# Performance work log

Hardware: AMD Instinct MI355X
Metric: run time of the kernel (lower is better)

The kernel has to match this reference:

```python
import jax, jax.numpy as jnp
import numpy as np

N, NFEAT, NHID, NCLASS = 8192, 128, 128, 40


def _init(key, shape, fan_in):
    return jax.random.normal(key, shape, jnp.float32) / np.sqrt(fan_in).astype(np.float32)


def setup_inputs() -> dict:
    ks = jax.random.split(jax.random.key(0), 8)
    return {
        "x": jax.random.normal(ks[0], (N, NFEAT), jnp.float32),
        # dense normalized adjacency: row-stochastic-ish positive matrix
        "adj": jax.random.uniform(ks[1], (N, N), jnp.float32) * (2.0 / N),
        "W_emb": _init(ks[2], (NFEAT, NHID), NFEAT),
        "b_emb": jnp.zeros((NHID,), jnp.float32),
        "W_gc1": _init(ks[3], (NHID, NHID), NHID),
        "b_gc1": jnp.zeros((NHID,), jnp.float32),
        "W_e": _init(ks[4], (2 * NHID, NHID), 2 * NHID),
        "b_e": jnp.zeros((NHID,), jnp.float32),
        "W_gc2": _init(ks[5], (NHID, NCLASS), NHID),
        "b_gc2": jnp.zeros((NCLASS,), jnp.float32),
        "fully_connected_graph": 1,  # unused by forward (passed but never read)
    }


def reference(x, adj, W_emb, b_emb, W_gc1, b_gc1, W_e, b_e, W_gc2, b_gc2,
              fully_connected_graph):
    nhid = W_emb.shape[1]
    # x = self.emb(x)
    h = x @ W_emb + b_emb  # [N, nhid]

    # Edge branch. Original materializes edge_feat[i*N+j] = concat(h[i], h[j])
    # ([N*N, 2*nhid]) then GraphConvolution_edge: support = edge_feat @ W_e,
    # reshaped [N, N, nhid], aggregated x_e[i] = sum_j adj[i,j] * support[i,j] + b_e.
    # Algebraically identical fused form (same math, no O(N^2*nhid) tensor):
    #   support[i,j] = h[i] @ W_e[:nhid] + h[j] @ W_e[nhid:]
    #   x_e[i] = deg[i] * (h[i] @ W_e_src) + (adj @ (h @ W_e_dst))[i] + b_e
    s_src = h @ W_e[:nhid]   # [N, nhid]
    s_dst = h @ W_e[nhid:]   # [N, nhid]
    deg = adj.sum(axis=1, keepdims=True)  # [N, 1] row sums
    x_e = deg * s_src + adj @ s_dst + b_e  # [N, nhid]

    # Node branch: gc1 -> relu -> dropout(eval: identity) -> gc2 -> log_softmax
    h1 = jax.nn.relu(adj @ (h @ W_gc1) + b_gc1)       # [N, nhid]
    logits = adj @ (h1 @ W_gc2) + b_gc2               # [N, nclass]
    out = jax.nn.log_softmax(logits, axis=1)
    return out, x_e
```

## Files before the change

kernel.cpp:

```cpp
#include <hip/hip_runtime.h>

#define DI __device__ __forceinline__

using f32x4  = __attribute__((ext_vector_type(4))) float;
using bf16x8 = __attribute__((ext_vector_type(8))) __bf16;
using u16x4  = __attribute__((ext_vector_type(4))) unsigned short;
using u32x4  = __attribute__((ext_vector_type(4))) unsigned int;

constexpr int NNODE = 8192;

DI unsigned short f2bf(float f) {
    unsigned int u = __builtin_bit_cast(unsigned int, f);
    u += 0x7fffu + ((u >> 16) & 1u);
    return (unsigned short)(u >> 16);
}
DI float bf2f(unsigned short s) {
    return __builtin_bit_cast(float, (unsigned int)s << 16);
}

DI int swz256(int r, int cb) { return r * 256 + (cb ^ ((r & 15) << 4)); }
DI int swz128(int r, int cb) { return r * 128 + (cb ^ ((r & 7) << 4)); }

__global__ void prep_w(const float* __restrict__ W_emb, const float* __restrict__ W_e,
                       const float* __restrict__ W_gc1, const float* __restrict__ W_gc2,
                       unsigned short* __restrict__ WembT_hi, unsigned short* __restrict__ WembT_lo,
                       unsigned short* __restrict__ WcatT_hi, unsigned short* __restrict__ WcatT_lo,
                       unsigned short* __restrict__ Wg2T_hi, unsigned short* __restrict__ Wg2T_lo)
{
    int gid = blockIdx.x * 256 + threadIdx.x;
    if (gid >= 576 * 128) return;
    int k = gid & 127, n = gid >> 7;
    float v;
    unsigned short *dh, *dl;
    if (n < 128) {
        v = W_emb[k * 128 + n];
        dh = WembT_hi + n * 128 + k; dl = WembT_lo + n * 128 + k;
    } else if (n < 512) {
        int m = n - 128;
        if (m < 128)      v = W_e[k * 128 + m];
        else if (m < 256) v = W_e[(k + 128) * 128 + (m - 128)];
        else              v = W_gc1[k * 128 + (m - 256)];
        dh = WcatT_hi + m * 128 + k; dl = WcatT_lo + m * 128 + k;
    } else {
        int c = n - 512;
        v = (c < 40) ? W_gc2[k * 40 + c] : 0.f;
        dh = Wg2T_hi + c * 128 + k; dl = Wg2T_lo + c * 128 + k;
    }
    unsigned short hi = f2bf(v);
    *dh = hi;
    *dl = f2bf(v - bf2f(hi));
}

template<int NCHUNK, int AKIND, int OUTKIND>
__global__ __launch_bounds__(256) void small_gemm(
    const float* __restrict__ Af32,
    const unsigned short* __restrict__ A_hi, const unsigned short* __restrict__ A_lo,
    const unsigned short* __restrict__ Bt_hi, const unsigned short* __restrict__ Bt_lo,
    const float* __restrict__ bias,
    unsigned short* __restrict__ out_hi, unsigned short* __restrict__ out_lo,
    float* __restrict__ out_s,
    unsigned short* __restrict__ out_t)
{
    __shared__ unsigned short Ah[64 * 128], Al[64 * 128];
    __shared__ unsigned short Bh[NCHUNK * 128], Bl[NCHUNK * 128];
    char* Ahc = (char*)Ah; char* Alc = (char*)Al;
    char* Bhc = (char*)Bh; char* Blc = (char*)Bl;

    const int tid = threadIdx.x;
    const int r0 = blockIdx.x * 64;
    const int n0 = blockIdx.y * NCHUNK;

    if constexpr (AKIND == 0) {
        #pragma unroll
        for (int p = 0; p < 8; ++p) {
            int idx = tid + 256 * p, r = idx >> 5, c4 = idx & 31;
            f32x4 v = *(const f32x4*)(Af32 + (size_t)(r0 + r) * 128 + c4 * 4);
            u16x4 ph, pl;
            #pragma unroll
            for (int j = 0; j < 4; ++j) {
                unsigned short hi = f2bf(v[j]);
                ph[j] = hi; pl[j] = f2bf(v[j] - bf2f(hi));
            }
            *(u16x4*)(Ahc + swz256(r, c4 * 8)) = ph;
            *(u16x4*)(Alc + swz256(r, c4 * 8)) = pl;
        }
    } else {
        #pragma unroll
        for (int p = 0; p < 4; ++p) {
            int idx = tid + 256 * p, r = idx >> 4, c = idx & 15;
            u32x4 vh = *(const u32x4*)(A_hi + (size_t)(r0 + r) * 128 + c * 8);
            u32x4 vl = *(const u32x4*)(A_lo + (size_t)(r0 + r) * 128 + c * 8);
            *(u32x4*)(Ahc + swz256(r, c * 16)) = vh;
            *(u32x4*)(Alc + swz256(r, c * 16)) = vl;
        }
    }
    #pragma unroll
    for (int p = 0; p < NCHUNK / 16; ++p) {
        int idx = tid + 256 * p, r = idx >> 4, c = idx & 15;
        u32x4 vh = *(const u32x4*)(Bt_hi + (size_t)(n0 + r) * 128 + c * 8);
        u32x4 vl = *(const u32x4*)(Bt_lo + (size_t)(n0 + r) * 128 + c * 8);
        *(u32x4*)(Bhc + swz256(r, c * 16)) = vh;
        *(u32x4*)(Blc + swz256(r, c * 16)) = vl;
    }
    __syncthreads();

    const int lane = tid & 63, wid = tid >> 6;
    const int lrow = lane & 15, lkb = (lane >> 4) * 16;
    constexpr int FN = NCHUNK / 16;
    f32x4 acc[FN];
    #pragma unroll
    for (int i = 0; i < FN; ++i) acc[i] = f32x4{0.f, 0.f, 0.f, 0.f};

    const int arow = wid * 16 + lrow;
    #pragma unroll
    for (int kk = 0; kk < 4; ++kk) {
        bf16x8 ah = *(const bf16x8*)(Ahc + swz256(arow, kk * 64 + lkb));
        bf16x8 al = *(const bf16x8*)(Alc + swz256(arow, kk * 64 + lkb));
        #pragma unroll
        for (int nf = 0; nf < FN; ++nf) {
            bf16x8 bh = *(const bf16x8*)(Bhc + swz256(nf * 16 + lrow, kk * 64 + lkb));
            bf16x8 bl = *(const bf16x8*)(Blc + swz256(nf * 16 + lrow, kk * 64 + lkb));
            acc[nf] = __builtin_amdgcn_mfma_f32_16x16x32_bf16(ah, bh, acc[nf], 0, 0, 0);
            acc[nf] = __builtin_amdgcn_mfma_f32_16x16x32_bf16(ah, bl, acc[nf], 0, 0, 0);
            acc[nf] = __builtin_amdgcn_mfma_f32_16x16x32_bf16(al, bh, acc[nf], 0, 0, 0);
        }
    }

    const int rowb = r0 + wid * 16 + ((lane >> 4) << 2);
    #pragma unroll
    for (int nf = 0; nf < FN; ++nf) {
        const int col = n0 + nf * 16 + lrow;
        if constexpr (OUTKIND == 0) {
            float bv = bias[col];
            #pragma unroll
            for (int j = 0; j < 4; ++j) {
                float v = acc[nf][j] + bv;
                unsigned short hi = f2bf(v);
                out_hi[(size_t)(rowb + j) * 128 + col] = hi;
                out_lo[(size_t)(rowb + j) * 128 + col] = f2bf(v - bf2f(hi));
            }
        } else if constexpr (OUTKIND == 1) {
            if (col < 128) {
                #pragma unroll
                for (int j = 0; j < 4; ++j)
                    out_s[(size_t)(rowb + j) * 128 + col] = acc[nf][j];
            } else {
                u16x4 pk = { f2bf(acc[nf][0]), f2bf(acc[nf][1]), f2bf(acc[nf][2]), f2bf(acc[nf][3]) };
                *(u16x4*)(out_t + (size_t)(col - 128) * NNODE + rowb) = pk;
            }
        } else {
            u16x4 pk = { f2bf(acc[nf][0]), f2bf(acc[nf][1]), f2bf(acc[nf][2]), f2bf(acc[nf][3]) };
            *(u16x4*)(out_t + (size_t)col * NNODE + rowb) = pk;
        }
    }
}

template<int NCOLS, bool DEG>
__global__ __launch_bounds__(512) void adj_gemm(
    const float* __restrict__ adj,
    const unsigned short* __restrict__ Bt,
    float* __restrict__ Tpart,
    float* __restrict__ deg)
{
    __shared__ unsigned short A_lds[2][64 * 64];
    __shared__ unsigned short B_lds[2][NCOLS * 64];

    const int tid = threadIdx.x;
    const int r0 = blockIdx.x * 64;
    const int ks = blockIdx.y;
    constexpr int KLEN = NNODE / 2;
    constexpr int NT = KLEN / 64;
    const int kbase = ks * KLEN;

    constexpr int NB = NCOLS / 64;
    f32x4 areg[2];
    u32x4 breg[NB];
    float dsum0 = 0.f, dsum1 = 0.f;
    const int ar0 = tid >> 4, ac4 = tid & 15;

    const int lane = tid & 63, wid = tid >> 6;
    constexpr int FM = (NCOLS == 256) ? 2 : 1;
    constexpr int FN = (NCOLS == 256) ? 4 : 2;
    const int wr = (NCOLS == 256) ? (wid >> 2) : (wid >> 1);
    const int wc = (NCOLS == 256) ? (wid & 3) : (wid & 1);
    const int row_w = wr * FM * 16, col_w = wc * FN * 16;
    const int lrow = lane & 15, lkb = (lane >> 4) * 16;

    f32x4 acc[FM][FN];
    #pragma unroll
    for (int fm = 0; fm < FM; ++fm)
        #pragma unroll
        for (int fn = 0; fn < FN; ++fn) acc[fm][fn] = f32x4{0.f, 0.f, 0.f, 0.f};

    auto loadG = [&](int t) {
        const int kt = kbase + t * 64;
        #pragma unroll
        for (int p = 0; p < 2; ++p) {
            areg[p] = *(const f32x4*)(adj + (size_t)(r0 + ar0 + 32 * p) * NNODE + kt + ac4 * 4);
            if (DEG) {
                float s = areg[p][0] + areg[p][1] + areg[p][2] + areg[p][3];
                if (p == 0) dsum0 += s; else dsum1 += s;
            }
        }
        #pragma unroll
        for (int p = 0; p < NB; ++p) {
            const int idx = tid + 512 * p, n = idx >> 3, c = idx & 7;
            breg[p] = *(const u32x4*)(Bt + (size_t)n * NNODE + kt + c * 8);
        }
    };
    auto storeL = [&](int buf) {
        char* Ac = (char*)(A_lds[buf]);
        char* Bc = (char*)(B_lds[buf]);
        #pragma unroll
        for (int p = 0; p < 2; ++p) {
            u16x4 pk = { f2bf(areg[p][0]), f2bf(areg[p][1]), f2bf(areg[p][2]), f2bf(areg[p][3]) };
            *(u16x4*)(Ac + swz128(ar0 + 32 * p, ac4 * 8)) = pk;
        }
        #pragma unroll
        for (int p = 0; p < NB; ++p) {
            const int idx = tid + 512 * p, n = idx >> 3, c = idx & 7;
            *(u32x4*)(Bc + swz128(n, c * 16)) = breg[p];
        }
    };

    loadG(0);
    storeL(0);
    for (int t = 0; t < NT; ++t) {
        if (t + 1 < NT) loadG(t + 1);
        __syncthreads();
        const char* Ac = (const char*)(A_lds[t & 1]);
        const char* Bc = (const char*)(B_lds[t & 1]);
        #pragma unroll
        for (int kk = 0; kk < 2; ++kk) {
            bf16x8 a[FM], b[FN];
            #pragma unroll
            for (int fm = 0; fm < FM; ++fm)
                a[fm] = *(const bf16x8*)(Ac + swz128(row_w + fm * 16 + lrow, kk * 64 + lkb));
            #pragma unroll
            for (int fn = 0; fn < FN; ++fn)
                b[fn] = *(const bf16x8*)(Bc + swz128(col_w + fn * 16 + lrow, kk * 64 + lkb));
            #pragma unroll
            for (int fm = 0; fm < FM; ++fm)
                #pragma unroll
                for (int fn = 0; fn < FN; ++fn)
                    acc[fm][fn] = __builtin_amdgcn_mfma_f32_16x16x32_bf16(a[fm], b[fn], acc[fm][fn], 0, 0, 0);
        }
        if (t + 1 < NT) storeL((t + 1) & 1);
    }

    float* outp = Tpart + (size_t)ks * NNODE * NCOLS;
    #pragma unroll
    for (int fm = 0; fm < FM; ++fm) {
        const int grow0 = r0 + row_w + fm * 16 + ((lane >> 4) << 2);
        #pragma unroll
        for (int fn = 0; fn < FN; ++fn) {
            const int gcol = col_w + fn * 16 + lrow;
            #pragma unroll
            for (int j = 0; j < 4; ++j)
                outp[(size_t)(grow0 + j) * NCOLS + gcol] = acc[fm][fn][j];
        }
    }

    if (DEG) {
        __syncthreads();
        float* sc = (float*)(&A_lds[0][0]);
        sc[tid] = dsum0;
        sc[512 + tid] = dsum1;
        __syncthreads();
        if (tid < 64) {
            const int base = (tid < 32) ? tid * 16 : (512 + (tid - 32) * 16);
            float s = 0.f;
            #pragma unroll
            for (int i = 0; i < 16; ++i) s += sc[base + i];
            atomicAdd(deg + r0 + tid, s);
        }
    }
}

__global__ void post1(const float* __restrict__ tA,
                      const float* __restrict__ s_src,
                      const float* __restrict__ deg,
                      const float* __restrict__ b_e,
                      const float* __restrict__ b_gc1,
                      float* __restrict__ x_e_out,
                      unsigned short* __restrict__ h1_hi, unsigned short* __restrict__ h1_lo)
{
    int gid = blockIdx.x * 256 + threadIdx.x;
    int i = gid >> 7, c = gid & 127;
    const size_t o = (size_t)i * 256;
    const size_t o2 = (size_t)NNODE * 256 + o;
    float t_sdst = tA[o + c] + tA[o2 + c];
    float t_g1   = tA[o + 128 + c] + tA[o2 + 128 + c];
    x_e_out[gid] = deg[i] * s_src[gid] + t_sdst + b_e[c];
    float h1 = t_g1 + b_gc1[c];
    h1 = h1 > 0.f ? h1 : 0.f;
    unsigned short hi = f2bf(h1);
    h1_hi[gid] = hi;
    h1_lo[gid] = f2bf(h1 - bf2f(hi));
}

__global__ void logsm(const float* __restrict__ tB,
                      const float* __restrict__ b_gc2,
                      float* __restrict__ out)
{
    const int wid = threadIdx.x >> 6, lane = threadIdx.x & 63;
    const int row = blockIdx.x * 4 + wid;
    float v = -1e30f;
    if (lane < 40)
        v = tB[(size_t)row * 64 + lane] + tB[(size_t)NNODE * 64 + (size_t)row * 64 + lane] + b_gc2[lane];
    float m = v;
    #pragma unroll
    for (int off = 32; off; off >>= 1) m = fmaxf(m, __shfl_xor(m, off, 64));
    float e = (lane < 40) ? expf(v - m) : 0.f;
    float s = e;
    #pragma unroll
    for (int off = 32; off; off >>= 1) s += __shfl_xor(s, off, 64);
    if (lane < 40) out[(size_t)row * 40 + lane] = v - m - logf(s);
}

extern "C" void kernel_launch(void* const* d_in, const int* in_sizes, int n_in,
                              void* d_out, int out_size, void* d_ws, size_t ws_size,
                              hipStream_t stream)
{
    const float* x     = (const float*)d_in[0];
    const float* adj   = (const float*)d_in[1];
    const float* W_emb = (const float*)d_in[2];
    const float* b_emb = (const float*)d_in[3];
    const float* W_gc1 = (const float*)d_in[4];
    const float* b_gc1 = (const float*)d_in[5];
    const float* W_e   = (const float*)d_in[6];
    const float* b_e   = (const float*)d_in[7];
    const float* W_gc2 = (const float*)d_in[8];
    const float* b_gc2 = (const float*)d_in[9];

    char* p = (char*)d_ws;
    auto take = [&](size_t bytes) { char* q = p; p += (bytes + 255) & ~(size_t)255; return q; };

    unsigned short* WembT_hi = (unsigned short*)take(128 * 128 * 2);
    unsigned short* WembT_lo = (unsigned short*)take(128 * 128 * 2);
    unsigned short* WcatT_hi = (unsigned short*)take(384 * 128 * 2);
    unsigned short* WcatT_lo = (unsigned short*)take(384 * 128 * 2);
    unsigned short* Wg2T_hi  = (unsigned short*)take(64 * 128 * 2);
    unsigned short* Wg2T_lo  = (unsigned short*)take(64 * 128 * 2);
    unsigned short* h_hi     = (unsigned short*)take((size_t)NNODE * 128 * 2);
    unsigned short* h_lo     = (unsigned short*)take((size_t)NNODE * 128 * 2);
    float*          s_src    = (float*)take((size_t)NNODE * 128 * 4);
    unsigned short* B_A      = (unsigned short*)take((size_t)256 * NNODE * 2);
    float*          tA       = (float*)take((size_t)2 * NNODE * 256 * 4);
    float*          deg      = (float*)take((size_t)NNODE * 4);
    unsigned short* B_B   = (unsigned short*)s_src;
    float*          tB    = tA;
    unsigned short* h1_hi = h_hi;
    unsigned short* h1_lo = h_lo;

    float* out_ls = (float*)d_out;
    float* x_e    = (float*)d_out + (size_t)NNODE * 40;

    hipMemsetAsync(deg, 0, NNODE * sizeof(float), stream);
    prep_w<<<288, 256, 0, stream>>>(W_emb, W_e, W_gc1, W_gc2,
                                    WembT_hi, WembT_lo, WcatT_hi, WcatT_lo, Wg2T_hi, Wg2T_lo);
    small_gemm<128, 0, 0><<<dim3(128, 1), 256, 0, stream>>>(
        x, nullptr, nullptr, WembT_hi, WembT_lo, b_emb, h_hi, h_lo, nullptr, nullptr);
    small_gemm<128, 1, 1><<<dim3(128, 3), 256, 0, stream>>>(
        nullptr, h_hi, h_lo, WcatT_hi, WcatT_lo, nullptr, nullptr, nullptr, s_src, B_A);
    adj_gemm<256, true><<<dim3(128, 2), 512, 0, stream>>>(adj, B_A, tA, deg);
    post1<<<4096, 256, 0, stream>>>(tA, s_src, deg, b_e, b_gc1, x_e, h1_hi, h1_lo);
    small_gemm<64, 1, 2><<<dim3(128, 1), 256, 0, stream>>>(
        nullptr, h1_hi, h1_lo, Wg2T_hi, Wg2T_lo, nullptr, nullptr, nullptr, nullptr, B_B);
    adj_gemm<64, false><<<dim3(128, 2), 512, 0, stream>>>(adj, B_B, tB, nullptr);
    logsm<<<2048, 256, 0, stream>>>(tB, b_gc2, out_ls);
}
```

Before: 160.7 us.

## Raise K-split in adjacency GEMMs and reverse second pass for cache reuse

The two adjacency GEMMs now split the K dimension into 4 and 8 slices instead of 2, launching 512 and 1024 blocks rather than 256 so more of the GPU's compute units are occupied. The second GEMM walks its K tiles in reverse order, so it starts on the adj region the first pass touched last, which may still be in cache. Launch bounds now also request 4 waves per SIMD. In exchange, more partial-sum buffers are written and then summed in the post-processing kernels, adding memory traffic and workspace.

New measurement: 164.5 us. 2.4% more time.

```diff
diff --git a/kernel.cpp b/kernel.cpp
--- a/kernel.cpp
+++ b/kernel.cpp
@@ -155,8 +155,8 @@
     }
 }
 
-template<int NCOLS, bool DEG>
-__global__ __launch_bounds__(512) void adj_gemm(
+template<int NCOLS, int KSPLIT, bool DEG, bool REV>
+__global__ __launch_bounds__(512, 4) void adj_gemm(
     const float* __restrict__ adj,
     const unsigned short* __restrict__ Bt,
     float* __restrict__ Tpart,
@@ -168,7 +168,7 @@
     const int tid = threadIdx.x;
     const int r0 = blockIdx.x * 64;
     const int ks = blockIdx.y;
-    constexpr int KLEN = NNODE / 2;
+    constexpr int KLEN = NNODE / KSPLIT;
     constexpr int NT = KLEN / 64;
     const int kbase = ks * KLEN;
 
@@ -192,6 +192,8 @@
         #pragma unroll
         for (int fn = 0; fn < FN; ++fn) acc[fm][fn] = f32x4{0.f, 0.f, 0.f, 0.f};
 
+    auto order = [&](int tt) { return REV ? (NT - 1 - tt) : tt; };
+
     auto loadG = [&](int t) {
         const int kt = kbase + t * 64;
         #pragma unroll
@@ -223,13 +225,13 @@
         }
     };
 
-    loadG(0);
+    loadG(order(0));
     storeL(0);
-    for (int t = 0; t < NT; ++t) {
-        if (t + 1 < NT) loadG(t + 1);
+    for (int tt = 0; tt < NT; ++tt) {
+        if (tt + 1 < NT) loadG(order(tt + 1));
         __syncthreads();
-        const char* Ac = (const char*)(A_lds[t & 1]);
-        const char* Bc = (const char*)(B_lds[t & 1]);
+        const char* Ac = (const char*)(A_lds[tt & 1]);
+        const char* Bc = (const char*)(B_lds[tt & 1]);
         #pragma unroll
         for (int kk = 0; kk < 2; ++kk) {
             bf16x8 a[FM], b[FN];
@@ -245,7 +247,7 @@
                 for (int fn = 0; fn < FN; ++fn)
                     acc[fm][fn] = __builtin_amdgcn_mfma_f32_16x16x32_bf16(a[fm], b[fn], acc[fm][fn], 0, 0, 0);
         }
-        if (t + 1 < NT) storeL((t + 1) & 1);
+        if (tt + 1 < NT) storeL((tt + 1) & 1);
     }
 
     float* outp = Tpart + (size_t)ks * NNODE * NCOLS;
@@ -277,6 +279,7 @@
     }
 }
 
+template<int KSPLIT>
 __global__ void post1(const float* __restrict__ tA,
                       const float* __restrict__ s_src,
                       const float* __restrict__ deg,
@@ -288,9 +291,13 @@
     int gid = blockIdx.x * 256 + threadIdx.x;
     int i = gid >> 7, c = gid & 127;
     const size_t o = (size_t)i * 256;
-    const size_t o2 = (size_t)NNODE * 256 + o;
-    float t_sdst = tA[o + c] + tA[o2 + c];
-    float t_g1   = tA[o + 128 + c] + tA[o2 + 128 + c];
+    float t_sdst = 0.f, t_g1 = 0.f;
+    #pragma unroll
+    for (int p = 0; p < KSPLIT; ++p) {
+        const size_t op = (size_t)p * NNODE * 256 + o;
+        t_sdst += tA[op + c];
+        t_g1   += tA[op + 128 + c];
+    }
     x_e_out[gid] = deg[i] * s_src[gid] + t_sdst + b_e[c];
     float h1 = t_g1 + b_gc1[c];
     h1 = h1 > 0.f ? h1 : 0.f;
@@ -299,6 +306,7 @@
     h1_lo[gid] = f2bf(h1 - bf2f(hi));
 }
 
+template<int KSPLIT>
 __global__ void logsm(const float* __restrict__ tB,
                       const float* __restrict__ b_gc2,
                       float* __restrict__ out)
@@ -306,8 +314,13 @@
     const int wid = threadIdx.x >> 6, lane = threadIdx.x & 63;
     const int row = blockIdx.x * 4 + wid;
     float v = -1e30f;
-    if (lane < 40)
-        v = tB[(size_t)row * 64 + lane] + tB[(size_t)NNODE * 64 + (size_t)row * 64 + lane] + b_gc2[lane];
+    if (lane < 40) {
+        float s = b_gc2[lane];
+        #pragma unroll
+        for (int p = 0; p < KSPLIT; ++p)
+            s += tB[(size_t)p * NNODE * 64 + (size_t)row * 64 + lane];
+        v = s;
+    }
     float m = v;
     #pragma unroll
     for (int off = 32; off; off >>= 1) m = fmaxf(m, __shfl_xor(m, off, 64));
@@ -333,6 +346,9 @@
     const float* W_gc2 = (const float*)d_in[8];
     const float* b_gc2 = (const float*)d_in[9];
 
+    constexpr int KSA = 4;
+    constexpr int KSB = 8;
+
     char* p = (char*)d_ws;
     auto take = [&](size_t bytes) { char* q = p; p += (bytes + 255) & ~(size_t)255; return q; };
 
@@ -346,7 +362,7 @@
     unsigned short* h_lo     = (unsigned short*)take((size_t)NNODE * 128 * 2);
     float*          s_src    = (float*)take((size_t)NNODE * 128 * 4);
     unsigned short* B_A      = (unsigned short*)take((size_t)256 * NNODE * 2);
-    float*          tA       = (float*)take((size_t)2 * NNODE * 256 * 4);
+    float*          tA       = (float*)take((size_t)KSA * NNODE * 256 * 4);
     float*          deg      = (float*)take((size_t)NNODE * 4);
     unsigned short* B_B   = (unsigned short*)s_src;
     float*          tB    = tA;
@@ -363,10 +379,10 @@
         x, nullptr, nullptr, WembT_hi, WembT_lo, b_emb, h_hi, h_lo, nullptr, nullptr);
     small_gemm<128, 1, 1><<<dim3(128, 3), 256, 0, stream>>>(
         nullptr, h_hi, h_lo, WcatT_hi, WcatT_lo, nullptr, nullptr, nullptr, s_src, B_A);
-    adj_gemm<256, true><<<dim3(128, 2), 512, 0, stream>>>(adj, B_A, tA, deg);
-    post1<<<4096, 256, 0, stream>>>(tA, s_src, deg, b_e, b_gc1, x_e, h1_hi, h1_lo);
+    adj_gemm<256, KSA, true, false><<<dim3(128, KSA), 512, 0, stream>>>(adj, B_A, tA, deg);
+    post1<KSA><<<4096, 256, 0, stream>>>(tA, s_src, deg, b_e, b_gc1, x_e, h1_hi, h1_lo);
     small_gemm<64, 1, 2><<<dim3(128, 1), 256, 0, stream>>>(
         nullptr, h1_hi, h1_lo, Wg2T_hi, Wg2T_lo, nullptr, nullptr, nullptr, nullptr, B_B);
-    adj_gemm<64, false><<<dim3(128, 2), 512, 0, stream>>>(adj, B_B, tB, nullptr);
-    logsm<<<2048, 256, 0, stream>>>(tB, b_gc2, out_ls);
-}
+    adj_gemm<64, KSB, false, true><<<dim3(128, KSB), 512, 0, stream>>>(adj, B_B, tB, nullptr);
+    logsm<KSB><<<2048, 256, 0, stream>>>(tB, b_gc2, out_ls);
+}
```

## Replace LDS-staged split-K adj GEMM with direct-register full-K tiles

Applied to the files above, without the earlier changes.

The adjacency GEMM no longer stages tiles through shared memory or splits K across two blocks. Each 32-row block streams adj and B straight from global memory into MFMA fragments, converting to bf16 in registers, and computes the degree with wave shuffles instead of atomics. The second adj pass walks K in reverse so it starts on the tail of adj still cached from the first pass. Dropping the split-K partial sums, the reduction reads and the memset is meant to cut overhead, at the cost of losing LDS reuse: each wave rereads B from global or cache with no software double-buffering.

Result: slower. 571.0 us (+255.3%).

```diff
diff --git a/kernel.cpp b/kernel.cpp
--- a/kernel.cpp
+++ b/kernel.cpp
@@ -19,7 +19,6 @@
 }
 
 DI int swz256(int r, int cb) { return r * 256 + (cb ^ ((r & 15) << 4)); }
-DI int swz128(int r, int cb) { return r * 128 + (cb ^ ((r & 7) << 4)); }
 
 __global__ void prep_w(const float* __restrict__ W_emb, const float* __restrict__ W_e,
                        const float* __restrict__ W_gc1, const float* __restrict__ W_gc2,
@@ -155,124 +154,96 @@
     }
 }
 
-template<int NCOLS, bool DEG>
-__global__ __launch_bounds__(512) void adj_gemm(
+template<int NCOLS, int WR, int WC, bool DEG, bool REV>
+__global__ __launch_bounds__(64 * WR * WC) void adj_gemm(
     const float* __restrict__ adj,
     const unsigned short* __restrict__ Bt,
-    float* __restrict__ Tpart,
+    float* __restrict__ T,
     float* __restrict__ deg)
 {
-    __shared__ unsigned short A_lds[2][64 * 64];
-    __shared__ unsigned short B_lds[2][NCOLS * 64];
-
-    const int tid = threadIdx.x;
-    const int r0 = blockIdx.x * 64;
-    const int ks = blockIdx.y;
-    constexpr int KLEN = NNODE / 2;
-    constexpr int NT = KLEN / 64;
-    const int kbase = ks * KLEN;
-
-    constexpr int NB = NCOLS / 64;
-    f32x4 areg[2];
-    u32x4 breg[NB];
-    float dsum0 = 0.f, dsum1 = 0.f;
-    const int ar0 = tid >> 4, ac4 = tid & 15;
-
+    constexpr int ROWS = 32;
+    constexpr int FM = ROWS / (16 * WR);
+    constexpr int FN = NCOLS / (16 * WC);
+    constexpr int NT = NNODE / 64;
+
+    const int tid  = threadIdx.x;
     const int lane = tid & 63, wid = tid >> 6;
-    constexpr int FM = (NCOLS == 256) ? 2 : 1;
-    constexpr int FN = (NCOLS == 256) ? 4 : 2;
-    const int wr = (NCOLS == 256) ? (wid >> 2) : (wid >> 1);
-    const int wc = (NCOLS == 256) ? (wid & 3) : (wid & 1);
-    const int row_w = wr * FM * 16, col_w = wc * FN * 16;
-    const int lrow = lane & 15, lkb = (lane >> 4) * 16;
+    const int wr = wid / WC, wc = wid % WC;
+    const int r0 = blockIdx.x * ROWS;
+    const int lrow = lane & 15;
+    const int lk8  = (lane >> 4) * 8;
+
+    const float* aptr = adj + (size_t)(r0 + wr * FM * 16 + lrow) * NNODE + lk8;
+    const int bcol0 = wc * FN * 16 + lrow;
 
     f32x4 acc[FM][FN];
     #pragma unroll
     for (int fm = 0; fm < FM; ++fm)
         #pragma unroll
         for (int fn = 0; fn < FN; ++fn) acc[fm][fn] = f32x4{0.f, 0.f, 0.f, 0.f};
-
-    auto loadG = [&](int t) {
-        const int kt = kbase + t * 64;
-        #pragma unroll
-        for (int p = 0; p < 2; ++p) {
-            areg[p] = *(const f32x4*)(adj + (size_t)(r0 + ar0 + 32 * p) * NNODE + kt + ac4 * 4);
-            if (DEG) {
-                float s = areg[p][0] + areg[p][1] + areg[p][2] + areg[p][3];
-                if (p == 0) dsum0 += s; else dsum1 += s;
-            }
-        }
-        #pragma unroll
-        for (int p = 0; p < NB; ++p) {
-            const int idx = tid + 512 * p, n = idx >> 3, c = idx & 7;
-            breg[p] = *(const u32x4*)(Bt + (size_t)n * NNODE + kt + c * 8);
-        }
-    };
-    auto storeL = [&](int buf) {
-        char* Ac = (char*)(A_lds[buf]);
-        char* Bc = (char*)(B_lds[buf]);
-        #pragma unroll
-        for (int p = 0; p < 2; ++p) {
-            u16x4 pk = { f2bf(areg[p][0]), f2bf(areg[p][1]), f2bf(areg[p][2]), f2bf(areg[p][3]) };
-            *(u16x4*)(Ac + swz128(ar0 + 32 * p, ac4 * 8)) = pk;
-        }
-        #pragma unroll
-        for (int p = 0; p < NB; ++p) {
-            const int idx = tid + 512 * p, n = idx >> 3, c = idx & 7;
-            *(u32x4*)(Bc + swz128(n, c * 16)) = breg[p];
-        }
-    };
-
-    loadG(0);
-    storeL(0);
-    for (int t = 0; t < NT; ++t) {
-        if (t + 1 < NT) loadG(t + 1);
-        __syncthreads();
-        const char* Ac = (const char*)(A_lds[t & 1]);
-        const char* Bc = (const char*)(B_lds[t & 1]);
+    float dsum[FM];
+    #pragma unroll
+    for (int fm = 0; fm < FM; ++fm) dsum[fm] = 0.f;
+
+    for (int tt = 0; tt < NT; ++tt) {
+        const int t = REV ? (NT - 1 - tt) : tt;
+        const int kt = t * 64;
+
+        f32x4 a[FM][2][2];
+        bf16x8 b[FN][2];
+        #pragma unroll
+        for (int fm = 0; fm < FM; ++fm)
+            #pragma unroll
+            for (int kk = 0; kk < 2; ++kk) {
+                const float* p = aptr + (size_t)fm * 16 * NNODE + kt + kk * 32;
+                a[fm][kk][0] = *(const f32x4*)(p);
+                a[fm][kk][1] = *(const f32x4*)(p + 4);
+            }
+        #pragma unroll
+        for (int fn = 0; fn < FN; ++fn)
+            #pragma unroll
+            for (int kk = 0; kk < 2; ++kk)
+                b[fn][kk] = *(const bf16x8*)(Bt + (size_t)(bcol0 + fn * 16) * NNODE + kt + kk * 32 + lk8);
+
         #pragma unroll
         for (int kk = 0; kk < 2; ++kk) {
-            bf16x8 a[FM], b[FN];
-            #pragma unroll
-            for (int fm = 0; fm < FM; ++fm)
-                a[fm] = *(const bf16x8*)(Ac + swz128(row_w + fm * 16 + lrow, kk * 64 + lkb));
-            #pragma unroll
-            for (int fn = 0; fn < FN; ++fn)
-                b[fn] = *(const bf16x8*)(Bc + swz128(col_w + fn * 16 + lrow, kk * 64 + lkb));
+            bf16x8 af[FM];
+            #pragma unroll
+            for (int fm = 0; fm < FM; ++fm) {
+                #pragma unroll
+                for (int j = 0; j < 8; ++j) {
+                    float v = (j < 4) ? a[fm][kk][0][j] : a[fm][kk][1][j - 4];
+                    af[fm][j] = __builtin_bit_cast(__bf16, f2bf(v));
+                    if (DEG && wc == 0) dsum[fm] += v;
+                }
+            }
             #pragma unroll
             for (int fm = 0; fm < FM; ++fm)
                 #pragma unroll
                 for (int fn = 0; fn < FN; ++fn)
-                    acc[fm][fn] = __builtin_amdgcn_mfma_f32_16x16x32_bf16(a[fm], b[fn], acc[fm][fn], 0, 0, 0);
-        }
-        if (t + 1 < NT) storeL((t + 1) & 1);
-    }
-
-    float* outp = Tpart + (size_t)ks * NNODE * NCOLS;
+                    acc[fm][fn] = __builtin_amdgcn_mfma_f32_16x16x32_bf16(af[fm], b[fn][kk], acc[fm][fn], 0, 0, 0);
+        }
+    }
+
     #pragma unroll
     for (int fm = 0; fm < FM; ++fm) {
-        const int grow0 = r0 + row_w + fm * 16 + ((lane >> 4) << 2);
+        const int grow0 = r0 + wr * FM * 16 + fm * 16 + ((lane >> 4) << 2);
         #pragma unroll
         for (int fn = 0; fn < FN; ++fn) {
-            const int gcol = col_w + fn * 16 + lrow;
+            const int gcol = wc * FN * 16 + fn * 16 + lrow;
             #pragma unroll
             for (int j = 0; j < 4; ++j)
-                outp[(size_t)(grow0 + j) * NCOLS + gcol] = acc[fm][fn][j];
-        }
-    }
-
-    if (DEG) {
-        __syncthreads();
-        float* sc = (float*)(&A_lds[0][0]);
-        sc[tid] = dsum0;
-        sc[512 + tid] = dsum1;
-        __syncthreads();
-        if (tid < 64) {
-            const int base = (tid < 32) ? tid * 16 : (512 + (tid - 32) * 16);
-            float s = 0.f;
-            #pragma unroll
-            for (int i = 0; i < 16; ++i) s += sc[base + i];
-            atomicAdd(deg + r0 + tid, s);
+                T[(size_t)(grow0 + j) * NCOLS + gcol] = acc[fm][fn][j];
+        }
+    }
+
+    if (DEG && wc == 0) {
+        #pragma unroll
+        for (int fm = 0; fm < FM; ++fm) {
+            float s = dsum[fm];
+            s += __shfl_xor(s, 16, 64);
+            s += __shfl_xor(s, 32, 64);
+            if (lane < 16) deg[r0 + wr * FM * 16 + fm * 16 + lane] = s;
         }
     }
 }
@@ -288,9 +259,8 @@
     int gid = blockIdx.x * 256 + threadIdx.x;
     int i = gid >> 7, c = gid & 127;
     const size_t o = (size_t)i * 256;
-    const size_t o2 = (size_t)NNODE * 256 + o;
-    float t_sdst = tA[o + c] + tA[o2 + c];
-    float t_g1   = tA[o + 128 + c] + tA[o2 + 128 + c];
+    float t_sdst = tA[o + c];
+    float t_g1   = tA[o + 128 + c];
     x_e_out[gid] = deg[i] * s_src[gid] + t_sdst + b_e[c];
     float h1 = t_g1 + b_gc1[c];
     h1 = h1 > 0.f ? h1 : 0.f;
@@ -307,7 +277,7 @@
     const int row = blockIdx.x * 4 + wid;
     float v = -1e30f;
     if (lane < 40)
-        v = tB[(size_t)row * 64 + lane] + tB[(size_t)NNODE * 64 + (size_t)row * 64 + lane] + b_gc2[lane];
+        v = tB[(size_t)row * 64 + lane] + b_gc2[lane];
     float m = v;
     #pragma unroll
     for (int off = 32; off; off >>= 1) m = fmaxf(m, __shfl_xor(m, off, 64));
@@ -346,7 +316,7 @@
     unsigned short* h_lo     = (unsigned short*)take((size_t)NNODE * 128 * 2);
     float*          s_src    = (float*)take((size_t)NNODE * 128 * 4);
     unsigned short* B_A      = (unsigned short*)take((size_t)256 * NNODE * 2);
-    float*          tA       = (float*)take((size_t)2 * NNODE * 256 * 4);
+    float*          tA       = (float*)take((size_t)NNODE * 256 * 4);
     float*          deg      = (float*)take((size_t)NNODE * 4);
     unsigned short* B_B   = (unsigned short*)s_src;
     float*          tB    = tA;
@@ -356,17 +326,16 @@
     float* out_ls = (float*)d_out;
     float* x_e    = (float*)d_out + (size_t)NNODE * 40;
 
-    hipMemsetAsync(deg, 0, NNODE * sizeof(float), stream);
     prep_w<<<288, 256, 0, stream>>>(W_emb, W_e, W_gc1, W_gc2,
                                     WembT_hi, WembT_lo, WcatT_hi, WcatT_lo, Wg2T_hi, Wg2T_lo);
     small_gemm<128, 0, 0><<<dim3(128, 1), 256, 0, stream>>>(
         x, nullptr, nullptr, WembT_hi, WembT_lo, b_emb, h_hi, h_lo, nullptr, nullptr);
     small_gemm<128, 1, 1><<<dim3(128, 3), 256, 0, stream>>>(
         nullptr, h_hi, h_lo, WcatT_hi, WcatT_lo, nullptr, nullptr, nullptr, s_src, B_A);
-    adj_gemm<256, true><<<dim3(128, 2), 512, 0, stream>>>(adj, B_A, tA, deg);
+    adj_gemm<256, 2, 4, true, false><<<256, 512, 0, stream>>>(adj, B_A, tA, deg);
     post1<<<4096, 256, 0, stream>>>(tA, s_src, deg, b_e, b_gc1, x_e, h1_hi, h1_lo);
     small_gemm<64, 1, 2><<<dim3(128, 1), 256, 0, stream>>>(
         nullptr, h1_hi, h1_lo, Wg2T_hi, Wg2T_lo, nullptr, nullptr, nullptr, nullptr, B_B);
-    adj_gemm<64, false><<<dim3(128, 2), 512, 0, stream>>>(adj, B_B, tB, nullptr);
+    adj_gemm<64, 2, 4, false, true><<<256, 512, 0, stream>>>(adj, B_B, tB, nullptr);
     logsm<<<2048, 256, 0, stream>>>(tB, b_gc2, out_ls);
 }
```
